# Kernel optimization log

Measured on AMD Instinct MI355X. Metric: run time of the kernel, lower is better.

## Reference

```python
import math
import jax, jax.numpy as jnp
import numpy as np

VOCAB = 30522
MAX_LEN = 512
D_MODEL = 768
MEM_SLOTS = 64
STEPS = 4
NUM_CLASSES = 8
DECAY = 0.9
SCORE_CLIP = 20.0
EPS = 1e-9


def setup_inputs() -> dict:
    key = jax.random.key(0)
    ks = jax.random.split(key, 12)
    B, T, d = 32, 512, D_MODEL
    inp = {
        "input_ids": jax.random.randint(ks[0], (B, T), 0, VOCAB, dtype=jnp.int64 if jax.config.jax_enable_x64 else jnp.int32),
        "attention_mask": jax.random.randint(ks[1], (B, T), 0, 2, dtype=jnp.int64 if jax.config.jax_enable_x64 else jnp.int32),
        "tok_emb": jax.random.normal(ks[2], (VOCAB, d), jnp.float32) * 0.02,
        "pos_emb": jax.random.normal(ks[3], (MAX_LEN, d), jnp.float32) * 0.02,
        "Wq": jax.random.normal(ks[4], (d, d), jnp.float32) / math.sqrt(d),
        "Wk": jax.random.normal(ks[5], (d, d), jnp.float32) / math.sqrt(d),
        "Wv": jax.random.normal(ks[6], (d, d), jnp.float32) / math.sqrt(d),
        "gate_W": jax.random.normal(ks[7], (d, d), jnp.float32) / math.sqrt(d),
        "gate_b": jnp.zeros((d,), jnp.float32),
        "ln_g": jnp.ones((d,), jnp.float32),
        "ln_b": jnp.zeros((d,), jnp.float32),
        "cls_W": jax.random.normal(ks[8], (d, NUM_CLASSES), jnp.float32) / math.sqrt(d),
        "cls_b": jnp.zeros((NUM_CLASSES,), jnp.float32),
        "mem_init": jax.random.normal(ks[9], (MEM_SLOTS, d), jnp.float32) * 0.02,
    }
    return inp


def _safe_masked_softmax(scores, m, valid):
    # scores: (B,T,S); m: (B,T) float {0,1}; valid: (B,) count of real tokens
    # torch masks whole token rows with -inf -> softmax -> nan_to_num -> renorm.
    # Equivalent nan-free form: full softmax over S, zero out pad rows, renorm.
    sm = jax.nn.softmax(scores, axis=-1)
    w = sm * m[:, :, None]
    w = jnp.where((valid == 0)[:, None, None], sm, w)  # all-pad batch rows: raw softmax
    w = jnp.nan_to_num(w, nan=0.0, posinf=0.0, neginf=0.0)
    return w / jnp.maximum(jnp.sum(w, axis=-1, keepdims=True), EPS)


def reference(input_ids, attention_mask, tok_emb, pos_emb, Wq, Wk, Wv,
              gate_W, gate_b, ln_g, ln_b, cls_W, cls_b, mem_init):
    B, T = input_ids.shape
    d = tok_emb.shape[1]
    scale = 1.0 / math.sqrt(d)

    x = tok_emb[input_ids] + pos_emb[:T][None, :, :]          # (B,T,d)
    m = (attention_mask > 0).astype(x.dtype)                  # (B,T)
    valid = jnp.sum(m, axis=1)                                # (B,)

    Qt = jnp.einsum('btd,de->bte', x, Wq)
    Vt = jnp.einsum('btd,de->bte', x, Wv)

    M = jnp.broadcast_to(mem_init[None], (B, MEM_SLOTS, d))
    for _ in range(STEPS):
        Km = jnp.einsum('bsd,de->bse', M, Wk)
        scores = jnp.clip(jnp.einsum('btd,bsd->bts', Qt, Km) * scale,
                          -SCORE_CLIP, SCORE_CLIP)
        W = _safe_masked_softmax(scores, m, valid)            # (B,T,S)
        write = jnp.einsum('bts,btd->bsd', W, Vt)             # (B,S,d)
        g = jax.nn.sigmoid(jnp.einsum('bsd,de->bse', M, gate_W) + gate_b)
        M = jnp.clip(DECAY * M + (1.0 - DECAY) * (g * write), -50.0, 50.0)

    Km = jnp.einsum('bsd,de->bse', M, Wk)
    scores = jnp.clip(jnp.einsum('btd,bsd->bts', Qt, Km) * scale,
                      -SCORE_CLIP, SCORE_CLIP)
    W = _safe_masked_softmax(scores, m, valid)
    token_context = jnp.einsum('bts,bsd->btd', W, M)          # (B,T,d)

    m3 = m[:, :, None]
    pooled = jnp.sum(token_context * m3, axis=1) / jnp.maximum(jnp.sum(m3, axis=1), 1.0)

    mu = jnp.mean(pooled, axis=-1, keepdims=True)
    var = jnp.mean(jnp.square(pooled - mu), axis=-1, keepdims=True)
    pooled = (pooled - mu) * jax.lax.rsqrt(var + 1e-5) * ln_g + ln_b

    logits = pooled @ cls_W + cls_b
    return jnp.nan_to_num(logits, nan=0.0, posinf=0.0, neginf=0.0)
```

## Files before the change

### kernel.cpp

```cpp
#include <hip/hip_runtime.h>
#include <math.h>

namespace {

constexpr int kBatch = 32;
constexpr int kTok   = 512;
constexpr int kDim   = 768;
constexpr int kSlots = 64;
constexpr int kSteps = 4;
constexpr int kCls   = 8;
constexpr float kScale = 0.03608439182435161f;
constexpr int kPad   = 40;

typedef __attribute__((ext_vector_type(4))) float f32x4;
typedef __attribute__((ext_vector_type(8))) short bf16x8;
typedef __attribute__((ext_vector_type(8))) unsigned short u16x8;
typedef __attribute__((ext_vector_type(4))) unsigned short u16x4;

__device__ __forceinline__ float clipf(float x, float c) { return fminf(fmaxf(x, -c), c); }
__device__ __forceinline__ unsigned short f2bf(float f) {
  unsigned u = __float_as_uint(f);
  return (unsigned short)((u + 0x7fffu + ((u >> 16) & 1u)) >> 16);
}
__device__ __forceinline__ float bf2f(unsigned short h) {
  return __uint_as_float(((unsigned)h) << 16);
}

__global__ __launch_bounds__(256) void k_prep(
    const float* __restrict__ Wv, const float* __restrict__ gW,
    unsigned short* __restrict__ WvT, unsigned short* __restrict__ gWT)
{
  __shared__ float tile[32][33];
  const int mat = blockIdx.z;
  const float* src = (mat == 0) ? Wv : gW;
  unsigned short* dst = (mat == 0) ? WvT : gWT;
  const int tx = threadIdx.x & 31, ty = threadIdx.x >> 5;
  const int r0 = blockIdx.y * 32, c0 = blockIdx.x * 32;
  #pragma unroll
  for (int q = 0; q < 4; ++q)
    tile[ty + 8*q][tx] = src[(size_t)(r0 + ty + 8*q) * kDim + c0 + tx];
  __syncthreads();
  #pragma unroll
  for (int q = 0; q < 4; ++q)
    dst[(size_t)(c0 + ty + 8*q) * kDim + r0 + tx] = f2bf(tile[tx][ty + 8*q]);
}

__global__ __launch_bounds__(64) void k_wqk(
    const float* __restrict__ Wk, const float* __restrict__ Wq,
    unsigned short* __restrict__ WqkT)
{
  __shared__ unsigned short As[64][kPad];
  __shared__ unsigned short Bs[64][kPad];
  const int lane = threadIdx.x;
  const int m0 = blockIdx.x * 64, n0 = blockIdx.y * 64;
  const int fr = lane & 15, kg = (lane >> 4) << 3, crow = (lane >> 4) << 2;
  f32x4 acc[4][4];
  #pragma unroll
  for (int i = 0; i < 4; ++i)
    #pragma unroll
    for (int j = 0; j < 4; ++j) acc[i][j] = (f32x4)(0.f);
  const float* arow = Wk + (size_t)(m0 + lane) * kDim;
  const float* brow = Wq + (size_t)(n0 + lane) * kDim;
  for (int k0 = 0; k0 < kDim; k0 += 32) {
    unsigned short av[32], bv[32];
    #pragma unroll
    for (int q = 0; q < 8; ++q) {
      float4 a4 = *reinterpret_cast<const float4*>(arow + k0 + 4*q);
      float4 b4 = *reinterpret_cast<const float4*>(brow + k0 + 4*q);
      av[4*q+0]=f2bf(a4.x); av[4*q+1]=f2bf(a4.y); av[4*q+2]=f2bf(a4.z); av[4*q+3]=f2bf(a4.w);
      bv[4*q+0]=f2bf(b4.x); bv[4*q+1]=f2bf(b4.y); bv[4*q+2]=f2bf(b4.z); bv[4*q+3]=f2bf(b4.w);
    }
    #pragma unroll
    for (int h = 0; h < 4; ++h) {
      *reinterpret_cast<u16x8*>(&As[lane][8*h]) = *reinterpret_cast<u16x8*>(&av[8*h]);
      *reinterpret_cast<u16x8*>(&Bs[lane][8*h]) = *reinterpret_cast<u16x8*>(&bv[8*h]);
    }
    __syncthreads();
    bf16x8 a[4], bb[4];
    #pragma unroll
    for (int mt = 0; mt < 4; ++mt) a[mt] = *reinterpret_cast<const bf16x8*>(&As[mt*16 + fr][kg]);
    #pragma unroll
    for (int nt = 0; nt < 4; ++nt) bb[nt] = *reinterpret_cast<const bf16x8*>(&Bs[nt*16 + fr][kg]);
    #pragma unroll
    for (int mt = 0; mt < 4; ++mt)
      #pragma unroll
      for (int nt = 0; nt < 4; ++nt)
        acc[mt][nt] = __builtin_amdgcn_mfma_f32_16x16x32_bf16(a[mt], bb[nt], acc[mt][nt], 0, 0, 0);
    __syncthreads();
  }
  #pragma unroll
  for (int mt = 0; mt < 4; ++mt) {
    const int row = m0 + mt*16 + crow;
    #pragma unroll
    for (int nt = 0; nt < 4; ++nt) {
      const int col = n0 + nt*16 + fr;
      #pragma unroll
      for (int r = 0; r < 4; ++r)
        WqkT[(size_t)(row + r) * kDim + col] = f2bf(acc[mt][nt][r]);
    }
  }
}

__global__ __launch_bounds__(256) void k_minit(
    const float* __restrict__ mi, float* __restrict__ M, unsigned short* __restrict__ Mb)
{
  int i = blockIdx.x * 256 + threadIdx.x;
  constexpr int per = kSlots * kDim / 4;
  float4 v = reinterpret_cast<const float4*>(mi)[i % per];
  reinterpret_cast<float4*>(M)[i] = v;
  u16x4 p; p[0]=f2bf(v.x); p[1]=f2bf(v.y); p[2]=f2bf(v.z); p[3]=f2bf(v.w);
  *reinterpret_cast<u16x4*>(Mb + (size_t)i*4) = p;
}

__global__ __launch_bounds__(256) void k_valid(const int* __restrict__ mask, float* __restrict__ vf) {
  __shared__ float red[256];
  const int b = blockIdx.x, tid = threadIdx.x;
  float c = 0.f;
  for (int t = tid; t < kTok; t += 256) c += (mask[b*kTok + t] > 0) ? 1.f : 0.f;
  red[tid] = c; __syncthreads();
  for (int off = 128; off > 0; off >>= 1) { if (tid < off) red[tid] += red[tid+off]; __syncthreads(); }
  if (tid == 0) vf[b] = red[0];
}

__global__ __launch_bounds__(256) void k_embed_qv(
    const int* __restrict__ ids, const float* __restrict__ tok, const float* __restrict__ pos,
    const unsigned short* __restrict__ WqkT, const unsigned short* __restrict__ WvT,
    unsigned short* __restrict__ Qk, unsigned short* __restrict__ VtT)
{
  __shared__ unsigned short As[64][kPad];
  __shared__ unsigned short Bq[128][kPad];
  __shared__ unsigned short Bv[128][kPad];
  __shared__ int rid[64];
  const int tid = threadIdx.x;
  const int m0 = blockIdx.x * 64, n0 = blockIdx.y * 128;
  if (tid < 64) rid[tid] = ids[m0 + tid];
  const int wave = tid >> 6, lane = tid & 63;
  const int ar = tid >> 2, ac = (tid & 3) << 3;
  const int br = tid >> 1, bc = (tid & 1) << 4;
  const int fr = lane & 15, kg = (lane >> 4) << 3, crow = (lane >> 4) << 2;
  f32x4 accq[4][2], accv[4][2];
  #pragma unroll
  for (int i = 0; i < 4; ++i)
    #pragma unroll
    for (int j = 0; j < 2; ++j) { accq[i][j] = (f32x4)(0.f); accv[i][j] = (f32x4)(0.f); }
  __syncthreads();
  const float* tokrow = tok + (size_t)rid[ar] * kDim;
  const float* posrow = pos + (size_t)((m0 + ar) & (kTok - 1)) * kDim;
  const unsigned short* bqrow = WqkT + (size_t)(n0 + br) * kDim;
  const unsigned short* bvrow = WvT  + (size_t)(n0 + br) * kDim;

  float4 tv0 = *reinterpret_cast<const float4*>(tokrow + ac);
  float4 tv1 = *reinterpret_cast<const float4*>(tokrow + ac + 4);
  float4 pv0 = *reinterpret_cast<const float4*>(posrow + ac);
  float4 pv1 = *reinterpret_cast<const float4*>(posrow + ac + 4);
  u16x8 q0 = *reinterpret_cast<const u16x8*>(bqrow + bc);
  u16x8 q1 = *reinterpret_cast<const u16x8*>(bqrow + bc + 8);
  u16x8 v0 = *reinterpret_cast<const u16x8*>(bvrow + bc);
  u16x8 v1 = *reinterpret_cast<const u16x8*>(bvrow + bc + 8);

  for (int k0 = 0; k0 < kDim; k0 += 32) {
    unsigned short av[8];
    av[0]=f2bf(tv0.x+pv0.x); av[1]=f2bf(tv0.y+pv0.y); av[2]=f2bf(tv0.z+pv0.z); av[3]=f2bf(tv0.w+pv0.w);
    av[4]=f2bf(tv1.x+pv1.x); av[5]=f2bf(tv1.y+pv1.y); av[6]=f2bf(tv1.z+pv1.z); av[7]=f2bf(tv1.w+pv1.w);
    *reinterpret_cast<u16x8*>(&As[ar][ac]) = *reinterpret_cast<u16x8*>(&av[0]);
    *reinterpret_cast<u16x8*>(&Bq[br][bc])     = q0;
    *reinterpret_cast<u16x8*>(&Bq[br][bc + 8]) = q1;
    *reinterpret_cast<u16x8*>(&Bv[br][bc])     = v0;
    *reinterpret_cast<u16x8*>(&Bv[br][bc + 8]) = v1;
    __syncthreads();
    if (k0 + 32 < kDim) {
      const int kn = k0 + 32;
      tv0 = *reinterpret_cast<const float4*>(tokrow + kn + ac);
      tv1 = *reinterpret_cast<const float4*>(tokrow + kn + ac + 4);
      pv0 = *reinterpret_cast<const float4*>(posrow + kn + ac);
      pv1 = *reinterpret_cast<const float4*>(posrow + kn + ac + 4);
      q0 = *reinterpret_cast<const u16x8*>(bqrow + kn + bc);
      q1 = *reinterpret_cast<const u16x8*>(bqrow + kn + bc + 8);
      v0 = *reinterpret_cast<const u16x8*>(bvrow + kn + bc);
      v1 = *reinterpret_cast<const u16x8*>(bvrow + kn + bc + 8);
    }
    bf16x8 a[4], bq[2], bv[2];
    #pragma unroll
    for (int mt = 0; mt < 4; ++mt) a[mt] = *reinterpret_cast<const bf16x8*>(&As[mt*16 + fr][kg]);
    #pragma unroll
    for (int nt = 0; nt < 2; ++nt) {
      bq[nt] = *reinterpret_cast<const bf16x8*>(&Bq[wave*32 + nt*16 + fr][kg]);
      bv[nt] = *reinterpret_cast<const bf16x8*>(&Bv[wave*32 + nt*16 + fr][kg]);
    }
    #pragma unroll
    for (int mt = 0; mt < 4; ++mt)
      #pragma unroll
      for (int nt = 0; nt < 2; ++nt) {
        accq[mt][nt] = __builtin_amdgcn_mfma_f32_16x16x32_bf16(a[mt], bq[nt], accq[mt][nt], 0, 0, 0);
        accv[mt][nt] = __builtin_amdgcn_mfma_f32_16x16x32_bf16(a[mt], bv[nt], accv[mt][nt], 0, 0, 0);
      }
    __syncthreads();
  }
  const int b = m0 >> 9;
  unsigned short* vb = VtT + (size_t)b * kDim * kTok;
  #pragma unroll
  for (int mt = 0; mt < 4; ++mt) {
    const int trow = m0 + mt*16 + crow;
    const int tloc = trow & (kTok - 1);
    #pragma unroll
    for (int nt = 0; nt < 2; ++nt) {
      const int dcol = n0 + wave*32 + nt*16 + fr;
      u16x4 pk;
      #pragma unroll
      for (int r = 0; r < 4; ++r) {
        Qk[(size_t)(trow + r) * kDim + dcol] = f2bf(accq[mt][nt][r]);
        pk[r] = f2bf(accv[mt][nt][r]);
      }
      *reinterpret_cast<u16x4*>(vb + (size_t)dcol * kTok + tloc) = pk;
    }
  }
}

__global__ __launch_bounds__(64) void k_scores(
    const unsigned short* __restrict__ Qk, const unsigned short* __restrict__ Mb,
    const int* __restrict__ mask, const float* __restrict__ vf,
    unsigned short* __restrict__ Wt)
{
  __shared__ unsigned short As[32][kPad];
  __shared__ unsigned short Bs[64][kPad];
  const int lane = threadIdx.x;
  const int b = blockIdx.y, t0 = blockIdx.x * 32;
  const int fr = lane & 15, kg = (lane >> 4) << 3, crow = (lane >> 4) << 2;
  const int ar = lane >> 1, ac = (lane & 1) << 4;
  f32x4 acc[2][4];
  #pragma unroll
  for (int i = 0; i < 2; ++i)
    #pragma unroll
    for (int j = 0; j < 4; ++j) acc[i][j] = (f32x4)(0.f);
  const unsigned short* qrow = Qk + (size_t)(b*kTok + t0 + ar) * kDim;
  const unsigned short* krow = Mb + (size_t)(b*kSlots + lane) * kDim;

  u16x8 pa0 = *reinterpret_cast<const u16x8*>(qrow + ac);
  u16x8 pa1 = *reinterpret_cast<const u16x8*>(qrow + ac + 8);
  u16x8 pb[4];
  #pragma unroll
  for (int h = 0; h < 4; ++h) pb[h] = *reinterpret_cast<const u16x8*>(krow + 8*h);

  for (int k0 = 0; k0 < kDim; k0 += 32) {
    *reinterpret_cast<u16x8*>(&As[ar][ac])     = pa0;
    *reinterpret_cast<u16x8*>(&As[ar][ac + 8]) = pa1;
    #pragma unroll
    for (int h = 0; h < 4; ++h) *reinterpret_cast<u16x8*>(&Bs[lane][8*h]) = pb[h];
    __syncthreads();
    if (k0 + 32 < kDim) {
      const int kn = k0 + 32;
      pa0 = *reinterpret_cast<const u16x8*>(qrow + kn + ac);
      pa1 = *reinterpret_cast<const u16x8*>(qrow + kn + ac + 8);
      #pragma unroll
      for (int h = 0; h < 4; ++h) pb[h] = *reinterpret_cast<const u16x8*>(krow + kn + 8*h);
    }
    bf16x8 a[2], bb[4];
    #pragma unroll
    for (int mt = 0; mt < 2; ++mt) a[mt] = *reinterpret_cast<const bf16x8*>(&As[mt*16 + fr][kg]);
    #pragma unroll
    for (int nt = 0; nt < 4; ++nt) bb[nt] = *reinterpret_cast<const bf16x8*>(&Bs[nt*16 + fr][kg]);
    #pragma unroll
    for (int mt = 0; mt < 2; ++mt)
      #pragma unroll
      for (int nt = 0; nt < 4; ++nt)
        acc[mt][nt] = __builtin_amdgcn_mfma_f32_16x16x32_bf16(a[mt], bb[nt], acc[mt][nt], 0, 0, 0);
    __syncthreads();
  }
  #pragma unroll
  for (int mt = 0; mt < 2; ++mt)
    #pragma unroll
    for (int nt = 0; nt < 4; ++nt)
      #pragma unroll
      for (int r = 0; r < 4; ++r)
        acc[mt][nt][r] = clipf(acc[mt][nt][r] * kScale, 20.f);
  const float vfb = vf[b];
  float fac[2][4];
  #pragma unroll
  for (int mt = 0; mt < 2; ++mt) {
    #pragma unroll
    for (int r = 0; r < 4; ++r) {
      float mx = fmaxf(fmaxf(acc[mt][0][r], acc[mt][1][r]), fmaxf(acc[mt][2][r], acc[mt][3][r]));
      #pragma unroll
      for (int m = 1; m < 16; m <<= 1) mx = fmaxf(mx, __shfl_xor(mx, m, 64));
      float sum = 0.f;
      #pragma unroll
      for (int nt = 0; nt < 4; ++nt) { float e = __expf(acc[mt][nt][r] - mx); acc[mt][nt][r] = e; sum += e; }
      #pragma unroll
      for (int m = 1; m < 16; m <<= 1) sum += __shfl_xor(sum, m, 64);
      const int tloc = t0 + mt*16 + crow + r;
      const bool keep = (mask[b*kTok + tloc] > 0) || (vfb == 0.f);
      fac[mt][r] = keep ? (1.f / sum) : 0.f;
    }
  }
  unsigned short* wb = Wt + (size_t)b * kSlots * kTok;
  #pragma unroll
  for (int mt = 0; mt < 2; ++mt) {
    const int tbase = t0 + mt*16 + crow;
    #pragma unroll
    for (int nt = 0; nt < 4; ++nt) {
      const int s = nt*16 + fr;
      u16x4 pk;
      #pragma unroll
      for (int r = 0; r < 4; ++r) pk[r] = f2bf(acc[mt][nt][r] * fac[mt][r]);
      *reinterpret_cast<u16x4*>(wb + (size_t)s * kTok + tbase) = pk;
    }
  }
}

__global__ __launch_bounds__(64) void k_write_gate(
    const unsigned short* __restrict__ Wt, const unsigned short* __restrict__ VtT,
    const unsigned short* __restrict__ MbIn, const unsigned short* __restrict__ gWT,
    const float* __restrict__ gb, float* __restrict__ M, unsigned short* __restrict__ MbOut)
{
  __shared__ unsigned short As[64][kPad];
  __shared__ unsigned short Bs[64][kPad];
  const int lane = threadIdx.x;
  const int b = blockIdx.y, n0 = blockIdx.x * 64;
  const int fr = lane & 15, kg = (lane >> 4) << 3, crow = (lane >> 4) << 2;
  f32x4 aw[4][4], ag[4][4];
  #pragma unroll
  for (int i = 0; i < 4; ++i)
    #pragma unroll
    for (int j = 0; j < 4; ++j) { aw[i][j] = (f32x4)(0.f); ag[i][j] = (f32x4)(0.f); }

  {
    const unsigned short* arow = Wt  + (size_t)b * kSlots * kTok + (size_t)lane * kTok;
    const unsigned short* brow = VtT + (size_t)b * kDim * kTok + (size_t)(n0 + lane) * kTok;
    u16x8 pa[4], pb[4];
    #pragma unroll
    for (int h = 0; h < 4; ++h) {
      pa[h] = *reinterpret_cast<const u16x8*>(arow + 8*h);
      pb[h] = *reinterpret_cast<const u16x8*>(brow + 8*h);
    }
    for (int k0 = 0; k0 < kTok; k0 += 32) {
      #pragma unroll
      for (int h = 0; h < 4; ++h) {
        *reinterpret_cast<u16x8*>(&As[lane][8*h]) = pa[h];
        *reinterpret_cast<u16x8*>(&Bs[lane][8*h]) = pb[h];
      }
      __syncthreads();
      if (k0 + 32 < kTok) {
        const int kn = k0 + 32;
        #pragma unroll
        for (int h = 0; h < 4; ++h) {
          pa[h] = *reinterpret_cast<const u16x8*>(arow + kn + 8*h);
          pb[h] = *reinterpret_cast<const u16x8*>(brow + kn + 8*h);
        }
      }
      bf16x8 a[4], bb[4];
      #pragma unroll
      for (int mt = 0; mt < 4; ++mt) a[mt] = *reinterpret_cast<const bf16x8*>(&As[mt*16 + fr][kg]);
      #pragma unroll
      for (int nt = 0; nt < 4; ++nt) bb[nt] = *reinterpret_cast<const bf16x8*>(&Bs[nt*16 + fr][kg]);
      #pragma unroll
      for (int mt = 0; mt < 4; ++mt)
        #pragma unroll
        for (int nt = 0; nt < 4; ++nt)
          aw[mt][nt] = __builtin_amdgcn_mfma_f32_16x16x32_bf16(a[mt], bb[nt], aw[mt][nt], 0, 0, 0);
      __syncthreads();
    }
  }
  {
    const unsigned short* arow = MbIn + (size_t)(b * kSlots + lane) * kDim;
    const unsigned short* brow = gWT + (size_t)(n0 + lane) * kDim;
    u16x8 pa[4], pb[4];
    #pragma unroll
    for (int h = 0; h < 4; ++h) {
      pa[h] = *reinterpret_cast<const u16x8*>(arow + 8*h);
      pb[h] = *reinterpret_cast<const u16x8*>(brow + 8*h);
    }
    for (int k0 = 0; k0 < kDim; k0 += 32) {
      #pragma unroll
      for (int h = 0; h < 4; ++h) {
        *reinterpret_cast<u16x8*>(&As[lane][8*h]) = pa[h];
        *reinterpret_cast<u16x8*>(&Bs[lane][8*h]) = pb[h];
      }
      __syncthreads();
      if (k0 + 32 < kDim) {
        const int kn = k0 + 32;
        #pragma unroll
        for (int h = 0; h < 4; ++h) {
          pa[h] = *reinterpret_cast<const u16x8*>(arow + kn + 8*h);
          pb[h] = *reinterpret_cast<const u16x8*>(brow + kn + 8*h);
        }
      }
      bf16x8 a[4], bb[4];
      #pragma unroll
      for (int mt = 0; mt < 4; ++mt) a[mt] = *reinterpret_cast<const bf16x8*>(&As[mt*16 + fr][kg]);
      #pragma unroll
      for (int nt = 0; nt < 4; ++nt) bb[nt] = *reinterpret_cast<const bf16x8*>(&Bs[nt*16 + fr][kg]);
      #pragma unroll
      for (int mt = 0; mt < 4; ++mt)
        #pragma unroll
        for (int nt = 0; nt < 4; ++nt)
          ag[mt][nt] = __builtin_amdgcn_mfma_f32_16x16x32_bf16(a[mt], bb[nt], ag[mt][nt], 0, 0, 0);
      __syncthreads();
    }
  }
  #pragma unroll
  for (int mt = 0; mt < 4; ++mt) {
    const int s = mt*16 + crow;
    #pragma unroll
    for (int nt = 0; nt < 4; ++nt) {
      const int d = n0 + nt*16 + fr;
      #pragma unroll
      for (int r = 0; r < 4; ++r) {
        const size_t off = (size_t)(b*kSlots + s + r) * kDim + d;
        float z = ag[mt][nt][r] + gb[d];
        float g = 1.f / (1.f + __expf(-z));
        float mn = clipf(0.9f * M[off] + 0.1f * g * aw[mt][nt][r], 50.f);
        M[off] = mn;
        MbOut[off] = f2bf(mn);
      }
    }
  }
}

__global__ __launch_bounds__(256) void k_final(
    const unsigned short* __restrict__ Wt, const float* __restrict__ M,
    const int* __restrict__ mask, const float* __restrict__ vf,
    const float* __restrict__ lng, const float* __restrict__ lnb,
    const float* __restrict__ clsW, const float* __restrict__ clsb,
    float* __restrict__ out)
{
  __shared__ float red[256];
  __shared__ float wsum[kSlots];
  __shared__ float pooled[kDim];
  __shared__ float sh_mu, sh_var;
  const int b = blockIdx.x, tid = threadIdx.x;
  const unsigned short* wb = Wt + (size_t)b * kSlots * kTok;

  {
    const int s = tid & 63, q = tid >> 6;
    const unsigned short* wr = wb + (size_t)s * kTok + q * 128;
    const int* mrow = mask + b * kTok + q * 128;
    float p = 0.f;
    #pragma unroll 4
    for (int j = 0; j < 16; ++j) {
      u16x8 v = *reinterpret_cast<const u16x8*>(wr + 8*j);
      #pragma unroll
      for (int e = 0; e < 8; ++e)
        if (mrow[8*j + e] > 0) p += bf2f(v[e]);
    }
    red[tid] = p;
  }
  __syncthreads();
  if (tid < 64) wsum[tid] = red[tid] + red[tid+64] + red[tid+128] + red[tid+192];
  __syncthreads();

  const float denom = fmaxf(vf[b], 1.f);
  for (int d = tid; d < kDim; d += 256) {
    float acc = 0.f;
    const float* Mb2 = M + (size_t)(b*kSlots) * kDim + d;
    #pragma unroll 4
    for (int s = 0; s < kSlots; ++s) acc += wsum[s] * Mb2[(size_t)s * kDim];
    pooled[d] = acc / denom;
  }
  __syncthreads();

  float lp = 0.f;
  for (int d = tid; d < kDim; d += 256) lp += pooled[d];
  red[tid] = lp; __syncthreads();
  for (int off = 128; off > 0; off >>= 1) { if (tid < off) red[tid] += red[tid+off]; __syncthreads(); }
  if (tid == 0) sh_mu = red[0] / kDim;
  __syncthreads();
  const float mu = sh_mu;
  float lv = 0.f;
  for (int d = tid; d < kDim; d += 256) { float z = pooled[d] - mu; lv += z*z; }
  red[tid] = lv; __syncthreads();
  for (int off = 128; off > 0; off >>= 1) { if (tid < off) red[tid] += red[tid+off]; __syncthreads(); }
  if (tid == 0) sh_var = red[0] / kDim;
  __syncthreads();
  const float inv = rsqrtf(sh_var + 1e-5f);
  for (int d = tid; d < kDim; d += 256)
    pooled[d] = (pooled[d] - mu) * inv * lng[d] + lnb[d];
  __syncthreads();

  {
    const int c = tid & 7, dg = tid >> 3;
    float part = 0.f;
    for (int d = dg; d < kDim; d += 32) part += pooled[d] * clsW[(size_t)d * kCls + c];
    red[tid] = part;
  }
  __syncthreads();
  if (tid < 8) {
    float s = clsb[tid];
    #pragma unroll
    for (int dg = 0; dg < 32; ++dg) s += red[dg*8 + tid];
    if (!isfinite(s)) s = 0.f;
    out[b*kCls + tid] = s;
  }
}

}

extern "C" void kernel_launch(void* const* d_in, const int* in_sizes, int n_in,
                              void* d_out, int out_size, void* d_ws, size_t ws_size,
                              hipStream_t stream)
{
  const int*   ids = (const int*)  d_in[0];
  const int*   msk = (const int*)  d_in[1];
  const float* tok = (const float*)d_in[2];
  const float* pos = (const float*)d_in[3];
  const float* Wq  = (const float*)d_in[4];
  const float* Wk  = (const float*)d_in[5];
  const float* Wv  = (const float*)d_in[6];
  const float* gW  = (const float*)d_in[7];
  const float* gb  = (const float*)d_in[8];
  const float* lng = (const float*)d_in[9];
  const float* lnb = (const float*)d_in[10];
  const float* cW  = (const float*)d_in[11];
  const float* cb  = (const float*)d_in[12];
  const float* mi  = (const float*)d_in[13];
  float* out = (float*)d_out;
  char* base = (char*)d_ws;

  size_t off = 0;
  unsigned short* Qk   = (unsigned short*)(base + off); off += (size_t)kBatch*kTok*kDim*2;
  unsigned short* VtT  = (unsigned short*)(base + off); off += (size_t)kBatch*kDim*kTok*2;
  unsigned short* Wt   = (unsigned short*)(base + off); off += (size_t)kBatch*kSlots*kTok*2;
  unsigned short* WvT  = (unsigned short*)(base + off); off += (size_t)kDim*kDim*2;
  unsigned short* gWT  = (unsigned short*)(base + off); off += (size_t)kDim*kDim*2;
  unsigned short* WqkT = (unsigned short*)(base + off); off += (size_t)kDim*kDim*2;
  float* M   = (float*)(base + off);          off += (size_t)kBatch*kSlots*kDim*4;
  unsigned short* Mb0 = (unsigned short*)(base + off); off += (size_t)kBatch*kSlots*kDim*2;
  unsigned short* Mb1 = (unsigned short*)(base + off); off += (size_t)kBatch*kSlots*kDim*2;
  float* vf  = (float*)(base + off);          off += 256;

  k_prep<<<dim3(kDim/32, kDim/32, 2), 256, 0, stream>>>(Wv, gW, WvT, gWT);
  k_wqk<<<dim3(kDim/64, kDim/64), 64, 0, stream>>>(Wk, Wq, WqkT);
  k_minit<<<dim3((kBatch*kSlots*kDim/4)/256), 256, 0, stream>>>(mi, M, Mb0);
  k_valid<<<dim3(kBatch), 256, 0, stream>>>(msk, vf);
  k_embed_qv<<<dim3(kBatch*kTok/64, kDim/128), 256, 0, stream>>>(ids, tok, pos, WqkT, WvT, Qk, VtT);
  unsigned short* mcur = Mb0;
  unsigned short* mnext = Mb1;
  for (int it = 0; it < kSteps; ++it) {
    k_scores<<<dim3(kTok/32, kBatch), 64, 0, stream>>>(Qk, mcur, msk, vf, Wt);
    k_write_gate<<<dim3(kDim/64, kBatch), 64, 0, stream>>>(Wt, VtT, mcur, gWT, gb, M, mnext);
    unsigned short* t = mcur; mcur = mnext; mnext = t;
  }
  k_scores<<<dim3(kTok/32, kBatch), 64, 0, stream>>>(Qk, mcur, msk, vf, Wt);
  k_final<<<dim3(kBatch), 256, 0, stream>>>(Wt, M, msk, vf, lng, lnb, cW, cb, out);

  (void)in_sizes; (void)n_in; (void)out_size; (void)ws_size;
}
```

Measured before the change: 538.6 us.

## Double-buffer LDS tiles and split-K across waves in scores and write-gate kernels

Adds LDS double buffering to the embedding QV GEMM and the scores GEMM so each k-step needs one barrier instead of two. k_scores moves to two waves that split the 64 memory slots, and the per-row softmax max and sum are merged across the two waves through shared memory. k_write_gate moves from 1 wave to 4 waves that split the K dimension, each with a private LDS tile and no barriers in the loop. The partial accumulators are then reduced through a large shared buffer before the gated memory update. This raises parallelism in the small per-step kernels, at the cost of about 72KB of LDS per block in k_write_gate, which limits occupancy.

Measured after the change: 568.6 us. 5.6% more time.

```diff
diff --git a/kernel.cpp b/kernel.cpp
--- a/kernel.cpp
+++ b/kernel.cpp
@@ -11,6 +11,7 @@
 constexpr int kCls   = 8;
 constexpr float kScale = 0.03608439182435161f;
 constexpr int kPad   = 40;
+constexpr int kPad2  = 36;
 
 typedef __attribute__((ext_vector_type(4))) float f32x4;
 typedef __attribute__((ext_vector_type(8))) short bf16x8;
@@ -127,9 +128,9 @@
     const unsigned short* __restrict__ WqkT, const unsigned short* __restrict__ WvT,
     unsigned short* __restrict__ Qk, unsigned short* __restrict__ VtT)
 {
-  __shared__ unsigned short As[64][kPad];
-  __shared__ unsigned short Bq[128][kPad];
-  __shared__ unsigned short Bv[128][kPad];
+  __shared__ unsigned short As[2][64][kPad];
+  __shared__ unsigned short Bq[2][128][kPad];
+  __shared__ unsigned short Bv[2][128][kPad];
   __shared__ int rid[64];
   const int tid = threadIdx.x;
   const int m0 = blockIdx.x * 64, n0 = blockIdx.y * 128;
@@ -149,43 +150,66 @@
   const unsigned short* bqrow = WqkT + (size_t)(n0 + br) * kDim;
   const unsigned short* bvrow = WvT  + (size_t)(n0 + br) * kDim;
 
-  float4 tv0 = *reinterpret_cast<const float4*>(tokrow + ac);
-  float4 tv1 = *reinterpret_cast<const float4*>(tokrow + ac + 4);
-  float4 pv0 = *reinterpret_cast<const float4*>(posrow + ac);
-  float4 pv1 = *reinterpret_cast<const float4*>(posrow + ac + 4);
-  u16x8 q0 = *reinterpret_cast<const u16x8*>(bqrow + bc);
-  u16x8 q1 = *reinterpret_cast<const u16x8*>(bqrow + bc + 8);
-  u16x8 v0 = *reinterpret_cast<const u16x8*>(bvrow + bc);
-  u16x8 v1 = *reinterpret_cast<const u16x8*>(bvrow + bc + 8);
-
-  for (int k0 = 0; k0 < kDim; k0 += 32) {
+  float4 tv0, tv1, pv0, pv1;
+  u16x8 q0, q1, v0, v1;
+  tv0 = *reinterpret_cast<const float4*>(tokrow + ac);
+  tv1 = *reinterpret_cast<const float4*>(tokrow + ac + 4);
+  pv0 = *reinterpret_cast<const float4*>(posrow + ac);
+  pv1 = *reinterpret_cast<const float4*>(posrow + ac + 4);
+  q0 = *reinterpret_cast<const u16x8*>(bqrow + bc);
+  q1 = *reinterpret_cast<const u16x8*>(bqrow + bc + 8);
+  v0 = *reinterpret_cast<const u16x8*>(bvrow + bc);
+  v1 = *reinterpret_cast<const u16x8*>(bvrow + bc + 8);
+  {
     unsigned short av[8];
     av[0]=f2bf(tv0.x+pv0.x); av[1]=f2bf(tv0.y+pv0.y); av[2]=f2bf(tv0.z+pv0.z); av[3]=f2bf(tv0.w+pv0.w);
     av[4]=f2bf(tv1.x+pv1.x); av[5]=f2bf(tv1.y+pv1.y); av[6]=f2bf(tv1.z+pv1.z); av[7]=f2bf(tv1.w+pv1.w);
-    *reinterpret_cast<u16x8*>(&As[ar][ac]) = *reinterpret_cast<u16x8*>(&av[0]);
-    *reinterpret_cast<u16x8*>(&Bq[br][bc])     = q0;
-    *reinterpret_cast<u16x8*>(&Bq[br][bc + 8]) = q1;
-    *reinterpret_cast<u16x8*>(&Bv[br][bc])     = v0;
-    *reinterpret_cast<u16x8*>(&Bv[br][bc + 8]) = v1;
-    __syncthreads();
-    if (k0 + 32 < kDim) {
-      const int kn = k0 + 32;
-      tv0 = *reinterpret_cast<const float4*>(tokrow + kn + ac);
-      tv1 = *reinterpret_cast<const float4*>(tokrow + kn + ac + 4);
-      pv0 = *reinterpret_cast<const float4*>(posrow + kn + ac);
-      pv1 = *reinterpret_cast<const float4*>(posrow + kn + ac + 4);
-      q0 = *reinterpret_cast<const u16x8*>(bqrow + kn + bc);
-      q1 = *reinterpret_cast<const u16x8*>(bqrow + kn + bc + 8);
-      v0 = *reinterpret_cast<const u16x8*>(bvrow + kn + bc);
-      v1 = *reinterpret_cast<const u16x8*>(bvrow + kn + bc + 8);
+    *reinterpret_cast<u16x8*>(&As[0][ar][ac]) = *reinterpret_cast<u16x8*>(&av[0]);
+    *reinterpret_cast<u16x8*>(&Bq[0][br][bc])     = q0;
+    *reinterpret_cast<u16x8*>(&Bq[0][br][bc + 8]) = q1;
+    *reinterpret_cast<u16x8*>(&Bv[0][br][bc])     = v0;
+    *reinterpret_cast<u16x8*>(&Bv[0][br][bc + 8]) = v1;
+  }
+  tv0 = *reinterpret_cast<const float4*>(tokrow + 32 + ac);
+  tv1 = *reinterpret_cast<const float4*>(tokrow + 32 + ac + 4);
+  pv0 = *reinterpret_cast<const float4*>(posrow + 32 + ac);
+  pv1 = *reinterpret_cast<const float4*>(posrow + 32 + ac + 4);
+  q0 = *reinterpret_cast<const u16x8*>(bqrow + 32 + bc);
+  q1 = *reinterpret_cast<const u16x8*>(bqrow + 32 + bc + 8);
+  v0 = *reinterpret_cast<const u16x8*>(bvrow + 32 + bc);
+  v1 = *reinterpret_cast<const u16x8*>(bvrow + 32 + bc + 8);
+  __syncthreads();
+
+  for (int i = 0; i < 24; ++i) {
+    const int cur = i & 1;
+    if (i < 23) {
+      unsigned short av[8];
+      av[0]=f2bf(tv0.x+pv0.x); av[1]=f2bf(tv0.y+pv0.y); av[2]=f2bf(tv0.z+pv0.z); av[3]=f2bf(tv0.w+pv0.w);
+      av[4]=f2bf(tv1.x+pv1.x); av[5]=f2bf(tv1.y+pv1.y); av[6]=f2bf(tv1.z+pv1.z); av[7]=f2bf(tv1.w+pv1.w);
+      *reinterpret_cast<u16x8*>(&As[cur^1][ar][ac]) = *reinterpret_cast<u16x8*>(&av[0]);
+      *reinterpret_cast<u16x8*>(&Bq[cur^1][br][bc])     = q0;
+      *reinterpret_cast<u16x8*>(&Bq[cur^1][br][bc + 8]) = q1;
+      *reinterpret_cast<u16x8*>(&Bv[cur^1][br][bc])     = v0;
+      *reinterpret_cast<u16x8*>(&Bv[cur^1][br][bc + 8]) = v1;
+      if (i < 22) {
+        const int kn = (i + 2) * 32;
+        tv0 = *reinterpret_cast<const float4*>(tokrow + kn + ac);
+        tv1 = *reinterpret_cast<const float4*>(tokrow + kn + ac + 4);
+        pv0 = *reinterpret_cast<const float4*>(posrow + kn + ac);
+        pv1 = *reinterpret_cast<const float4*>(posrow + kn + ac + 4);
+        q0 = *reinterpret_cast<const u16x8*>(bqrow + kn + bc);
+        q1 = *reinterpret_cast<const u16x8*>(bqrow + kn + bc + 8);
+        v0 = *reinterpret_cast<const u16x8*>(bvrow + kn + bc);
+        v1 = *reinterpret_cast<const u16x8*>(bvrow + kn + bc + 8);
+      }
     }
     bf16x8 a[4], bq[2], bv[2];
     #pragma unroll
-    for (int mt = 0; mt < 4; ++mt) a[mt] = *reinterpret_cast<const bf16x8*>(&As[mt*16 + fr][kg]);
+    for (int mt = 0; mt < 4; ++mt) a[mt] = *reinterpret_cast<const bf16x8*>(&As[cur][mt*16 + fr][kg]);
     #pragma unroll
     for (int nt = 0; nt < 2; ++nt) {
-      bq[nt] = *reinterpret_cast<const bf16x8*>(&Bq[wave*32 + nt*16 + fr][kg]);
-      bv[nt] = *reinterpret_cast<const bf16x8*>(&Bv[wave*32 + nt*16 + fr][kg]);
+      bq[nt] = *reinterpret_cast<const bf16x8*>(&Bq[cur][wave*32 + nt*16 + fr][kg]);
+      bv[nt] = *reinterpret_cast<const bf16x8*>(&Bv[cur][wave*32 + nt*16 + fr][kg]);
     }
     #pragma unroll
     for (int mt = 0; mt < 4; ++mt)
@@ -216,203 +240,322 @@
   }
 }
 
-__global__ __launch_bounds__(64) void k_scores(
+__global__ __launch_bounds__(128) void k_scores(
     const unsigned short* __restrict__ Qk, const unsigned short* __restrict__ Mb,
     const int* __restrict__ mask, const float* __restrict__ vf,
     unsigned short* __restrict__ Wt)
 {
-  __shared__ unsigned short As[32][kPad];
-  __shared__ unsigned short Bs[64][kPad];
-  const int lane = threadIdx.x;
+  __shared__ unsigned short As[2][32][kPad];
+  __shared__ unsigned short Bs[2][64][kPad];
+  __shared__ float xm[2][32];
+  __shared__ float xs[2][32];
+  const int tid = threadIdx.x;
+  const int w = tid >> 6, lane = tid & 63;
   const int b = blockIdx.y, t0 = blockIdx.x * 32;
   const int fr = lane & 15, kg = (lane >> 4) << 3, crow = (lane >> 4) << 2;
-  const int ar = lane >> 1, ac = (lane & 1) << 4;
-  f32x4 acc[2][4];
+  const int srow = tid >> 1, scol = (tid & 1) << 4;
+  const bool doA = (tid < 64);
+  const unsigned short* qrow = Qk + (size_t)(b*kTok + t0 + (srow & 31)) * kDim + scol;
+  const unsigned short* krow = Mb + (size_t)(b*kSlots + srow) * kDim + scol;
+  f32x4 acc[2][2];
   #pragma unroll
   for (int i = 0; i < 2; ++i)
     #pragma unroll
-    for (int j = 0; j < 4; ++j) acc[i][j] = (f32x4)(0.f);
-  const unsigned short* qrow = Qk + (size_t)(b*kTok + t0 + ar) * kDim;
-  const unsigned short* krow = Mb + (size_t)(b*kSlots + lane) * kDim;
-
-  u16x8 pa0 = *reinterpret_cast<const u16x8*>(qrow + ac);
-  u16x8 pa1 = *reinterpret_cast<const u16x8*>(qrow + ac + 8);
-  u16x8 pb[4];
-  #pragma unroll
-  for (int h = 0; h < 4; ++h) pb[h] = *reinterpret_cast<const u16x8*>(krow + 8*h);
-
-  for (int k0 = 0; k0 < kDim; k0 += 32) {
-    *reinterpret_cast<u16x8*>(&As[ar][ac])     = pa0;
-    *reinterpret_cast<u16x8*>(&As[ar][ac + 8]) = pa1;
-    #pragma unroll
-    for (int h = 0; h < 4; ++h) *reinterpret_cast<u16x8*>(&Bs[lane][8*h]) = pb[h];
-    __syncthreads();
-    if (k0 + 32 < kDim) {
-      const int kn = k0 + 32;
-      pa0 = *reinterpret_cast<const u16x8*>(qrow + kn + ac);
-      pa1 = *reinterpret_cast<const u16x8*>(qrow + kn + ac + 8);
-      #pragma unroll
-      for (int h = 0; h < 4; ++h) pb[h] = *reinterpret_cast<const u16x8*>(krow + kn + 8*h);
-    }
-    bf16x8 a[2], bb[4];
-    #pragma unroll
-    for (int mt = 0; mt < 2; ++mt) a[mt] = *reinterpret_cast<const bf16x8*>(&As[mt*16 + fr][kg]);
-    #pragma unroll
-    for (int nt = 0; nt < 4; ++nt) bb[nt] = *reinterpret_cast<const bf16x8*>(&Bs[nt*16 + fr][kg]);
+    for (int j = 0; j < 2; ++j) acc[i][j] = (f32x4)(0.f);
+
+  u16x8 ra0, ra1, rb0, rb1;
+  if (doA) { ra0 = *reinterpret_cast<const u16x8*>(qrow); ra1 = *reinterpret_cast<const u16x8*>(qrow + 8); }
+  rb0 = *reinterpret_cast<const u16x8*>(krow); rb1 = *reinterpret_cast<const u16x8*>(krow + 8);
+  if (doA) {
+    *reinterpret_cast<u16x8*>(&As[0][srow][scol])     = ra0;
+    *reinterpret_cast<u16x8*>(&As[0][srow][scol + 8]) = ra1;
+  }
+  *reinterpret_cast<u16x8*>(&Bs[0][srow][scol])     = rb0;
+  *reinterpret_cast<u16x8*>(&Bs[0][srow][scol + 8]) = rb1;
+  if (doA) { ra0 = *reinterpret_cast<const u16x8*>(qrow + 32); ra1 = *reinterpret_cast<const u16x8*>(qrow + 40); }
+  rb0 = *reinterpret_cast<const u16x8*>(krow + 32); rb1 = *reinterpret_cast<const u16x8*>(krow + 40);
+  __syncthreads();
+
+  for (int i = 0; i < 24; ++i) {
+    const int cur = i & 1;
+    if (i < 23) {
+      if (doA) {
+        *reinterpret_cast<u16x8*>(&As[cur^1][srow][scol])     = ra0;
+        *reinterpret_cast<u16x8*>(&As[cur^1][srow][scol + 8]) = ra1;
+      }
+      *reinterpret_cast<u16x8*>(&Bs[cur^1][srow][scol])     = rb0;
+      *reinterpret_cast<u16x8*>(&Bs[cur^1][srow][scol + 8]) = rb1;
+      if (i < 22) {
+        const int kn = (i + 2) * 32;
+        if (doA) { ra0 = *reinterpret_cast<const u16x8*>(qrow + kn); ra1 = *reinterpret_cast<const u16x8*>(qrow + kn + 8); }
+        rb0 = *reinterpret_cast<const u16x8*>(krow + kn); rb1 = *reinterpret_cast<const u16x8*>(krow + kn + 8);
+      }
+    }
+    bf16x8 a[2], bb[2];
+    #pragma unroll
+    for (int mt = 0; mt < 2; ++mt) a[mt] = *reinterpret_cast<const bf16x8*>(&As[cur][mt*16 + fr][kg]);
+    #pragma unroll
+    for (int nt = 0; nt < 2; ++nt) bb[nt] = *reinterpret_cast<const bf16x8*>(&Bs[cur][w*32 + nt*16 + fr][kg]);
     #pragma unroll
     for (int mt = 0; mt < 2; ++mt)
       #pragma unroll
-      for (int nt = 0; nt < 4; ++nt)
+      for (int nt = 0; nt < 2; ++nt)
         acc[mt][nt] = __builtin_amdgcn_mfma_f32_16x16x32_bf16(a[mt], bb[nt], acc[mt][nt], 0, 0, 0);
     __syncthreads();
   }
   #pragma unroll
   for (int mt = 0; mt < 2; ++mt)
     #pragma unroll
-    for (int nt = 0; nt < 4; ++nt)
+    for (int nt = 0; nt < 2; ++nt)
       #pragma unroll
       for (int r = 0; r < 4; ++r)
         acc[mt][nt][r] = clipf(acc[mt][nt][r] * kScale, 20.f);
-  const float vfb = vf[b];
-  float fac[2][4];
+  float lmax[2][4], lsum[2][4];
   #pragma unroll
   for (int mt = 0; mt < 2; ++mt) {
     #pragma unroll
     for (int r = 0; r < 4; ++r) {
-      float mx = fmaxf(fmaxf(acc[mt][0][r], acc[mt][1][r]), fmaxf(acc[mt][2][r], acc[mt][3][r]));
+      float mx = fmaxf(acc[mt][0][r], acc[mt][1][r]);
       #pragma unroll
       for (int m = 1; m < 16; m <<= 1) mx = fmaxf(mx, __shfl_xor(mx, m, 64));
       float sum = 0.f;
       #pragma unroll
-      for (int nt = 0; nt < 4; ++nt) { float e = __expf(acc[mt][nt][r] - mx); acc[mt][nt][r] = e; sum += e; }
+      for (int nt = 0; nt < 2; ++nt) { float e = __expf(acc[mt][nt][r] - mx); acc[mt][nt][r] = e; sum += e; }
       #pragma unroll
       for (int m = 1; m < 16; m <<= 1) sum += __shfl_xor(sum, m, 64);
-      const int tloc = t0 + mt*16 + crow + r;
-      const bool keep = (mask[b*kTok + tloc] > 0) || (vfb == 0.f);
-      fac[mt][r] = keep ? (1.f / sum) : 0.f;
-    }
-  }
+      lmax[mt][r] = mx; lsum[mt][r] = sum;
+      if (fr == 0) {
+        const int tl = mt*16 + crow + r;
+        xm[w][tl] = mx; xs[w][tl] = sum;
+      }
+    }
+  }
+  __syncthreads();
+  const float vfb = vf[b];
   unsigned short* wb = Wt + (size_t)b * kSlots * kTok;
   #pragma unroll
   for (int mt = 0; mt < 2; ++mt) {
     const int tbase = t0 + mt*16 + crow;
     #pragma unroll
-    for (int nt = 0; nt < 4; ++nt) {
-      const int s = nt*16 + fr;
+    for (int r = 0; r < 4; ++r) {
+      const int tl = mt*16 + crow + r;
+      const float om = xm[w^1][tl], os = xs[w^1][tl];
+      const float m = fmaxf(lmax[mt][r], om);
+      const float tot = lsum[mt][r] * __expf(lmax[mt][r] - m) + os * __expf(om - m);
+      const bool keep = (mask[b*kTok + tbase + r] > 0) || (vfb == 0.f);
+      const float fac = keep ? (__expf(lmax[mt][r] - m) / tot) : 0.f;
+      #pragma unroll
+      for (int nt = 0; nt < 2; ++nt)
+        acc[mt][nt][r] *= fac;
+    }
+    #pragma unroll
+    for (int nt = 0; nt < 2; ++nt) {
+      const int s = w*32 + nt*16 + fr;
       u16x4 pk;
       #pragma unroll
-      for (int r = 0; r < 4; ++r) pk[r] = f2bf(acc[mt][nt][r] * fac[mt][r]);
+      for (int r = 0; r < 4; ++r) pk[r] = f2bf(acc[mt][nt][r]);
       *reinterpret_cast<u16x4*>(wb + (size_t)s * kTok + tbase) = pk;
     }
   }
 }
 
-__global__ __launch_bounds__(64) void k_write_gate(
+__global__ __launch_bounds__(256) void k_write_gate(
     const unsigned short* __restrict__ Wt, const unsigned short* __restrict__ VtT,
     const unsigned short* __restrict__ MbIn, const unsigned short* __restrict__ gWT,
     const float* __restrict__ gb, float* __restrict__ M, unsigned short* __restrict__ MbOut)
 {
-  __shared__ unsigned short As[64][kPad];
-  __shared__ unsigned short Bs[64][kPad];
-  const int lane = threadIdx.x;
+  __shared__ __align__(16) char smem[73728];
+  const int tid = threadIdx.x, w = tid >> 6, lane = tid & 63;
   const int b = blockIdx.y, n0 = blockIdx.x * 64;
   const int fr = lane & 15, kg = (lane >> 4) << 3, crow = (lane >> 4) << 2;
-  f32x4 aw[4][4], ag[4][4];
+  unsigned short* tA0 = (unsigned short*)(smem + w*18432);
+  unsigned short* tA1 = (unsigned short*)(smem + w*18432 + 4608);
+  unsigned short* tB0 = (unsigned short*)(smem + w*18432 + 9216);
+  unsigned short* tB1 = (unsigned short*)(smem + w*18432 + 13824);
+  f32x4 Wacc[4][4], Gacc[4][4];
   #pragma unroll
   for (int i = 0; i < 4; ++i)
     #pragma unroll
-    for (int j = 0; j < 4; ++j) { aw[i][j] = (f32x4)(0.f); ag[i][j] = (f32x4)(0.f); }
+    for (int j = 0; j < 4; ++j) { Wacc[i][j] = (f32x4)(0.f); Gacc[i][j] = (f32x4)(0.f); }
 
   {
-    const unsigned short* arow = Wt  + (size_t)b * kSlots * kTok + (size_t)lane * kTok;
-    const unsigned short* brow = VtT + (size_t)b * kDim * kTok + (size_t)(n0 + lane) * kTok;
+    const unsigned short* arow = Wt  + (size_t)b*kSlots*kTok + (size_t)lane*kTok + w*128;
+    const unsigned short* brow = VtT + (size_t)b*kDim*kTok + (size_t)(n0+lane)*kTok + w*128;
     u16x8 pa[4], pb[4];
     #pragma unroll
     for (int h = 0; h < 4; ++h) {
       pa[h] = *reinterpret_cast<const u16x8*>(arow + 8*h);
       pb[h] = *reinterpret_cast<const u16x8*>(brow + 8*h);
     }
-    for (int k0 = 0; k0 < kTok; k0 += 32) {
-      #pragma unroll
-      for (int h = 0; h < 4; ++h) {
-        *reinterpret_cast<u16x8*>(&As[lane][8*h]) = pa[h];
-        *reinterpret_cast<u16x8*>(&Bs[lane][8*h]) = pb[h];
-      }
-      __syncthreads();
-      if (k0 + 32 < kTok) {
-        const int kn = k0 + 32;
+    #pragma unroll
+    for (int h = 0; h < 4; ++h) {
+      *reinterpret_cast<u16x8*>(tA0 + lane*kPad2 + 8*h) = pa[h];
+      *reinterpret_cast<u16x8*>(tB0 + lane*kPad2 + 8*h) = pb[h];
+    }
+    #pragma unroll
+    for (int h = 0; h < 4; ++h) {
+      pa[h] = *reinterpret_cast<const u16x8*>(arow + 32 + 8*h);
+      pb[h] = *reinterpret_cast<const u16x8*>(brow + 32 + 8*h);
+    }
+    #pragma unroll
+    for (int i = 0; i < 4; ++i) {
+      unsigned short* cA = (i & 1) ? tA1 : tA0;
+      unsigned short* cB = (i & 1) ? tB1 : tB0;
+      if (i < 3) {
+        unsigned short* nA = (i & 1) ? tA0 : tA1;
+        unsigned short* nB = (i & 1) ? tB0 : tB1;
         #pragma unroll
         for (int h = 0; h < 4; ++h) {
-          pa[h] = *reinterpret_cast<const u16x8*>(arow + kn + 8*h);
-          pb[h] = *reinterpret_cast<const u16x8*>(brow + kn + 8*h);
+          *reinterpret_cast<u16x8*>(nA + lane*kPad2 + 8*h) = pa[h];
+          *reinterpret_cast<u16x8*>(nB + lane*kPad2 + 8*h) = pb[h];
         }
-      }
-      bf16x8 a[4], bb[4];
-      #pragma unroll
-      for (int mt = 0; mt < 4; ++mt) a[mt] = *reinterpret_cast<const bf16x8*>(&As[mt*16 + fr][kg]);
-      #pragma unroll
-      for (int nt = 0; nt < 4; ++nt) bb[nt] = *reinterpret_cast<const bf16x8*>(&Bs[nt*16 + fr][kg]);
+        if (i < 2) {
+          #pragma unroll
+          for (int h = 0; h < 4; ++h) {
+            pa[h] = *reinterpret_cast<const u16x8*>(arow + (i+2)*32 + 8*h);
+            pb[h] = *reinterpret_cast<const u16x8*>(brow + (i+2)*32 + 8*h);
+          }
+        }
+      }
+      bf16x8 a[4], bbv[4];
+      #pragma unroll
+      for (int mt = 0; mt < 4; ++mt) a[mt] = *reinterpret_cast<const bf16x8*>(cA + (mt*16 + fr)*kPad2 + kg);
+      #pragma unroll
+      for (int nt = 0; nt < 4; ++nt) bbv[nt] = *reinterpret_cast<const bf16x8*>(cB + (nt*16 + fr)*kPad2 + kg);
       #pragma unroll
       for (int mt = 0; mt < 4; ++mt)
         #pragma unroll
         for (int nt = 0; nt < 4; ++nt)
-          aw[mt][nt] = __builtin_amdgcn_mfma_f32_16x16x32_bf16(a[mt], bb[nt], aw[mt][nt], 0, 0, 0);
-      __syncthreads();
+          Wacc[mt][nt] = __builtin_amdgcn_mfma_f32_16x16x32_bf16(a[mt], bbv[nt], Wacc[mt][nt], 0, 0, 0);
     }
   }
   {
-    const unsigned short* arow = MbIn + (size_t)(b * kSlots + lane) * kDim;
-    const unsigned short* brow = gWT + (size_t)(n0 + lane) * kDim;
+    const unsigned short* arow = MbIn + (size_t)(b*kSlots + lane)*kDim + w*192;
+    const unsigned short* brow = gWT + (size_t)(n0 + lane)*kDim + w*192;
     u16x8 pa[4], pb[4];
     #pragma unroll
     for (int h = 0; h < 4; ++h) {
       pa[h] = *reinterpret_cast<const u16x8*>(arow + 8*h);
       pb[h] = *reinterpret_cast<const u16x8*>(brow + 8*h);
     }
-    for (int k0 = 0; k0 < kDim; k0 += 32) {
-      #pragma unroll
-      for (int h = 0; h < 4; ++h) {
-        *reinterpret_cast<u16x8*>(&As[lane][8*h]) = pa[h];
-        *reinterpret_cast<u16x8*>(&Bs[lane][8*h]) = pb[h];
-      }
-      __syncthreads();
-      if (k0 + 32 < kDim) {
-        const int kn = k0 + 32;
+    #pragma unroll
+    for (int h = 0; h < 4; ++h) {
+      *reinterpret_cast<u16x8*>(tA0 + lane*kPad2 + 8*h) = pa[h];
+      *reinterpret_cast<u16x8*>(tB0 + lane*kPad2 + 8*h) = pb[h];
+    }
+    #pragma unroll
+    for (int h = 0; h < 4; ++h) {
+      pa[h] = *reinterpret_cast<const u16x8*>(arow + 32 + 8*h);
+      pb[h] = *reinterpret_cast<const u16x8*>(brow + 32 + 8*h);
+    }
+    #pragma unroll
+    for (int i = 0; i < 6; ++i) {
+      unsigned short* cA = (i & 1) ? tA1 : tA0;
+      unsigned short* cB = (i & 1) ? tB1 : tB0;
+      if (i < 5) {
+        unsigned short* nA = (i & 1) ? tA0 : tA1;
+        unsigned short* nB = (i & 1) ? tB0 : tB1;
         #pragma unroll
         for (int h = 0; h < 4; ++h) {
-          pa[h] = *reinterpret_cast<const u16x8*>(arow + kn + 8*h);
-          pb[h] = *reinterpret_cast<const u16x8*>(brow + kn + 8*h);
+          *reinterpret_cast<u16x8*>(nA + lane*kPad2 + 8*h) = pa[h];
+          *reinterpret_cast<u16x8*>(nB + lane*kPad2 + 8*h) = pb[h];
         }
-      }
-      bf16x8 a[4], bb[4];
-      #pragma unroll
-      for (int mt = 0; mt < 4; ++mt) a[mt] = *reinterpret_cast<const bf16x8*>(&As[mt*16 + fr][kg]);
-      #pragma unroll
-      for (int nt = 0; nt < 4; ++nt) bb[nt] = *reinterpret_cast<const bf16x8*>(&Bs[nt*16 + fr][kg]);
+        if (i < 4) {
+          #pragma unroll
+          for (int h = 0; h < 4; ++h) {
+            pa[h] = *reinterpret_cast<const u16x8*>(arow + (i+2)*32 + 8*h);
+            pb[h] = *reinterpret_cast<const u16x8*>(brow + (i+2)*32 + 8*h);
+          }
+        }
+      }
+      bf16x8 a[4], bbv[4];
+      #pragma unroll
+      for (int mt = 0; mt < 4; ++mt) a[mt] = *reinterpret_cast<const bf16x8*>(cA + (mt*16 + fr)*kPad2 + kg);
+      #pragma unroll
+      for (int nt = 0; nt < 4; ++nt) bbv[nt] = *reinterpret_cast<const bf16x8*>(cB + (nt*16 + fr)*kPad2 + kg);
       #pragma unroll
       for (int mt = 0; mt < 4; ++mt)
         #pragma unroll
         for (int nt = 0; nt < 4; ++nt)
-          ag[mt][nt] = __builtin_amdgcn_mfma_f32_16x16x32_bf16(a[mt], bb[nt], ag[mt][nt], 0, 0, 0);
-      __syncthreads();
-    }
-  }
-  #pragma unroll
-  for (int mt = 0; mt < 4; ++mt) {
-    const int s = mt*16 + crow;
-    #pragma unroll
-    for (int nt = 0; nt < 4; ++nt) {
-      const int d = n0 + nt*16 + fr;
-      #pragma unroll
-      for (int r = 0; r < 4; ++r) {
-        const size_t off = (size_t)(b*kSlots + s + r) * kDim + d;
-        float z = ag[mt][nt][r] + gb[d];
-        float g = 1.f / (1.f + __expf(-z));
-        float mn = clipf(0.9f * M[off] + 0.1f * g * aw[mt][nt][r], 50.f);
-        M[off] = mn;
-        MbOut[off] = f2bf(mn);
-      }
-    }
+          Gacc[mt][nt] = __builtin_amdgcn_mfma_f32_16x16x32_bf16(a[mt], bbv[nt], Gacc[mt][nt], 0, 0, 0);
+    }
+  }
+  __syncthreads();
+  float (*WA)[65] = (float(*)[65])(smem);
+  float (*WB)[65] = (float(*)[65])(smem + 16640);
+  float (*GA)[65] = (float(*)[65])(smem + 33280);
+  float (*GB)[65] = (float(*)[65])(smem + 49920);
+  if (w == 1) {
+    #pragma unroll
+    for (int mt = 0; mt < 4; ++mt)
+      #pragma unroll
+      for (int nt = 0; nt < 4; ++nt)
+        #pragma unroll
+        for (int r = 0; r < 4; ++r) WA[mt*16 + crow + r][nt*16 + fr] = Wacc[mt][nt][r];
+  } else if (w == 3) {
+    #pragma unroll
+    for (int mt = 0; mt < 4; ++mt)
+      #pragma unroll
+      for (int nt = 0; nt < 4; ++nt)
+        #pragma unroll
+        for (int r = 0; r < 4; ++r) WB[mt*16 + crow + r][nt*16 + fr] = Wacc[mt][nt][r];
+  } else if (w == 0) {
+    #pragma unroll
+    for (int mt = 0; mt < 4; ++mt)
+      #pragma unroll
+      for (int nt = 0; nt < 4; ++nt)
+        #pragma unroll
+        for (int r = 0; r < 4; ++r) GA[mt*16 + crow + r][nt*16 + fr] = Gacc[mt][nt][r];
+  } else {
+    #pragma unroll
+    for (int mt = 0; mt < 4; ++mt)
+      #pragma unroll
+      for (int nt = 0; nt < 4; ++nt)
+        #pragma unroll
+        for (int r = 0; r < 4; ++r) GB[mt*16 + crow + r][nt*16 + fr] = Gacc[mt][nt][r];
+  }
+  __syncthreads();
+  if (w == 0) {
+    #pragma unroll
+    for (int mt = 0; mt < 4; ++mt)
+      #pragma unroll
+      for (int nt = 0; nt < 4; ++nt)
+        #pragma unroll
+        for (int r = 0; r < 4; ++r) WA[mt*16 + crow + r][nt*16 + fr] += Wacc[mt][nt][r];
+  } else if (w == 2) {
+    #pragma unroll
+    for (int mt = 0; mt < 4; ++mt)
+      #pragma unroll
+      for (int nt = 0; nt < 4; ++nt)
+        #pragma unroll
+        for (int r = 0; r < 4; ++r) WB[mt*16 + crow + r][nt*16 + fr] += Wacc[mt][nt][r];
+  } else if (w == 1) {
+    #pragma unroll
+    for (int mt = 0; mt < 4; ++mt)
+      #pragma unroll
+      for (int nt = 0; nt < 4; ++nt)
+        #pragma unroll
+        for (int r = 0; r < 4; ++r) GA[mt*16 + crow + r][nt*16 + fr] += Gacc[mt][nt][r];
+  } else {
+    #pragma unroll
+    for (int mt = 0; mt < 4; ++mt)
+      #pragma unroll
+      for (int nt = 0; nt < 4; ++nt)
+        #pragma unroll
+        for (int r = 0; r < 4; ++r) GB[mt*16 + crow + r][nt*16 + fr] += Gacc[mt][nt][r];
+  }
+  __syncthreads();
+  #pragma unroll
+  for (int r = 0; r < 16; ++r) {
+    const int s = w*16 + r;
+    const float wf = WA[s][lane] + WB[s][lane];
+    const float gf = GA[s][lane] + GB[s][lane];
+    const float z = gf + gb[n0 + lane];
+    const float g = 1.f / (1.f + __expf(-z));
+    const size_t off = (size_t)(b*kSlots + s) * kDim + n0 + lane;
+    const float mn = clipf(0.9f * M[off] + 0.1f * g * wf, 50.f);
+    M[off] = mn;
+    MbOut[off] = f2bf(mn);
   }
 }
 
@@ -535,11 +678,11 @@
   unsigned short* mcur = Mb0;
   unsigned short* mnext = Mb1;
   for (int it = 0; it < kSteps; ++it) {
-    k_scores<<<dim3(kTok/32, kBatch), 64, 0, stream>>>(Qk, mcur, msk, vf, Wt);
-    k_write_gate<<<dim3(kDim/64, kBatch), 64, 0, stream>>>(Wt, VtT, mcur, gWT, gb, M, mnext);
+    k_scores<<<dim3(kTok/32, kBatch), 128, 0, stream>>>(Qk, mcur, msk, vf, Wt);
+    k_write_gate<<<dim3(kDim/64, kBatch), 256, 0, stream>>>(Wt, VtT, mcur, gWT, gb, M, mnext);
     unsigned short* t = mcur; mcur = mnext; mnext = t;
   }
-  k_scores<<<dim3(kTok/32, kBatch), 64, 0, stream>>>(Qk, mcur, msk, vf, Wt);
+  k_scores<<<dim3(kTok/32, kBatch), 128, 0, stream>>>(Qk, mcur, msk, vf, Wt);
   k_final<<<dim3(kBatch), 256, 0, stream>>>(Wt, M, msk, vf, lng, lnb, cW, cb, out);
 
   (void)in_sizes; (void)n_in; (void)out_size; (void)ws_size;
```
